# Kernel optimization log

Measured on AMD Instinct MI355X. Metric: run time of the kernel, lower is better.

## Reference

```python
import jax, jax.numpy as jnp
import numpy as np
import math

B, QL, KL, H, QD, KD, VD = 4, 1024, 1024, 16, 1024, 1024, 1024
QH = QD // H  # 64
KH = KD // H  # 64


def setup_inputs() -> dict:
    rng = jax.random.key(0)
    ks = jax.random.split(rng, 8)
    return {
        "query": jax.random.normal(ks[0], (B, QL, QD), jnp.float32),
        "key": jax.random.normal(ks[1], (B, KL, KD), jnp.float32),
        "value": jax.random.normal(ks[2], (B, KL, VD), jnp.float32),
        "pad_mask": jax.random.randint(ks[3], (B, QL), 0, 2),
        "q_w": jax.random.uniform(ks[4], (H, QL, QH), jnp.float32),
        "k_w": jax.random.uniform(ks[5], (H, KL, KH), jnp.float32),
        "v_w": jax.random.uniform(ks[6], (H, KL, KH), jnp.float32),
        "o_w": jax.random.uniform(ks[7], (H * KH, QD), jnp.float32),
    }


def reference(query, key, value, pad_mask, q_w, k_w, v_w, o_w):
    b = query.shape[0]
    h, ql, qh = q_w.shape
    kl, kh = k_w.shape[1], k_w.shape[2]

    # mask construction: causal (triu, offset 1) OR pad mask tiled as in torch repeat+view
    causal = jnp.triu(jnp.ones((ql, kl), jnp.float32), 1) == 1            # [i, j]
    pad = jnp.tile(pad_mask, (1, kl)).reshape(b, ql, kl) == 1             # [b, i, j]
    mask = causal[None, :, :] | pad                                      # [b, i, j]

    # positional per-head projections: free index of input feature dim is summed out
    wq = jnp.einsum('biq,his->bhis', query, q_w)                          # [b, h, i, s]
    wk = jnp.einsum('bjk,hjt->bhjt', key, k_w)                            # [b, h, j, t]
    wv = jnp.einsum('bjv,hjt->bhjt', value, v_w)                          # [b, h, j, t]

    scale = math.sqrt(h)  # torch uses query.size()[1] == head_num after projection
    scores = jnp.einsum('bhis,bhjs->bhij', wq, wk) / scale                # [b, h, i, j]
    scores = jnp.where(mask[:, None, :, :], -jnp.inf, scores)
    scores = jnp.nan_to_num(scores)  # -inf -> finfo.min, matching torch.nan_to_num

    weight = jax.nn.softmax(scores, axis=0)  # unusual: softmax over the batch axis
    heads = jnp.einsum('bhij,bhjt->bhit', weight, wv)                     # [b, h, i, t]
    heads = heads.reshape(b, -1, h * kh)  # torch .view: reinterprets [h,i,t] as [i, h*t]
    return jnp.einsum('bit,to->bio', heads, o_w)                          # [b, i, q_dim]
```

## Files before the change

### kernel.cpp

```cpp
#include <hip/hip_runtime.h>
#include <hip/hip_bf16.h>

#define NB 4
#define NL 1024
#define NH 16
#define ND 1024
#define HD 64
#define FMIN_F32 (-3.4028234663852886e38f)
#define LOG2E 1.4426950408889634f

typedef __bf16 bf16x8 __attribute__((ext_vector_type(8)));
typedef float f32x4 __attribute__((ext_vector_type(4)));
typedef unsigned int u32;

static __device__ inline unsigned short f2bf(float f) {
    __hip_bfloat16 h = __float2bfloat16(f);
    return __builtin_bit_cast(unsigned short, h);
}

static __device__ inline void bfsplit(float x, unsigned short& hi, unsigned short& lo) {
    unsigned u = __builtin_bit_cast(unsigned, x);
    unsigned r = (u + 0x7FFFu + ((u >> 16) & 1u)) >> 16;
    hi = (unsigned short)r;
    float hf = __builtin_bit_cast(float, r << 16);
    lo = f2bf(x - hf);
}

static __device__ __forceinline__ void gload16(void* lds, const void* g) {
    __builtin_amdgcn_global_load_lds(
        (const __attribute__((address_space(1))) u32*)g,
        (__attribute__((address_space(3))) u32*)lds, 16, 0, 0);
}

__global__ __launch_bounds__(256)
void rowsum_kernel(const float* __restrict__ q, const float* __restrict__ k,
                   const float* __restrict__ v, float* __restrict__ out) {
    int gw   = blockIdx.x * 4 + (threadIdx.x >> 6);
    int lane = threadIdx.x & 63;
    int tensor = gw >> 12;
    int row    = gw & 4095;
    const float* src = tensor == 0 ? q : (tensor == 1 ? k : v);
    const float* p = src + (size_t)row * ND;
    float s = 0.f;
#pragma unroll
    for (int t = 0; t < 4; ++t) {
        float4 x = *reinterpret_cast<const float4*>(p + t * 256 + lane * 4);
        s += (x.x + x.y) + (x.z + x.w);
    }
#pragma unroll
    for (int off = 32; off; off >>= 1) s += __shfl_xor(s, off);
    if (lane == 0) out[tensor * (NB * NL) + row] = s;
}

__global__ __launch_bounds__(256)
void prep_kernel(const float* __restrict__ k_w, const float* __restrict__ v_w,
                 const float* __restrict__ o_w, const float* __restrict__ sums,
                 unsigned short* __restrict__ kPhi, unsigned short* __restrict__ kPlo,
                 unsigned short* __restrict__ vP, unsigned short* __restrict__ BP,
                 float* __restrict__ S) {
    __shared__ float tile[64][132];
    __shared__ float vsL[256];
    const int tid = threadIdx.x;
    const int bx  = blockIdx.x;
    if (bx < 256) {
        const int h = bx >> 4, jt = bx & 15;
        char* hiT = (char*)kPhi + (size_t)(h * 16 + jt) * 8192;
        char* loT = (char*)kPlo + (size_t)(h * 16 + jt) * 8192;
        const int row = tid >> 2;
        const int s0  = (tid & 3) * 16;
        const float* src = k_w + ((size_t)(h * NL + jt * 64 + row)) * HD + s0;
#pragma unroll
        for (int t = 0; t < 4; ++t) {
            float4 x = reinterpret_cast<const float4*>(src)[t];
            unsigned short h0, h1, h2, h3, l0, l1, l2, l3;
            bfsplit(x.x, h0, l0); bfsplit(x.y, h1, l1);
            bfsplit(x.z, h2, l2); bfsplit(x.w, h3, l3);
            int off = (row * 128 + (s0 + 4 * t) * 2) ^ ((row & 7) << 4);
            *(uint2*)(hiT + off) = make_uint2((u32)h0 | ((u32)h1 << 16),
                                              (u32)h2 | ((u32)h3 << 16));
            *(uint2*)(loT + off) = make_uint2((u32)l0 | ((u32)l1 << 16),
                                              (u32)l2 | ((u32)l3 << 16));
        }
    } else if (bx < 512) {
        const int h = (bx - 256) >> 4, jt = (bx - 256) & 15;
#pragma unroll
        for (int t = 0; t < 4; ++t) {
            int id = tid + 256 * t;
            int j = id >> 4, t4 = (id & 15) * 4;
            *(float4*)&tile[j][t4] =
                *(const float4*)(v_w + ((size_t)(h * NL + jt * 64 + j)) * HD + t4);
        }
        vsL[tid] = sums[2 * NB * NL + (tid >> 6) * NL + jt * 64 + (tid & 63)];
        __syncthreads();
        char* vT_ = (char*)vP + (size_t)(h * 16 + jt) * 8192;
        const int trow = tid >> 2;
        const int jq   = (tid & 3) * 16;
#pragma unroll
        for (int q = 0; q < 4; ++q) {
            int j4 = jq + 4 * q;
            uint2 u;
            u.x = (u32)f2bf(tile[j4 + 0][trow]) | ((u32)f2bf(tile[j4 + 1][trow]) << 16);
            u.y = (u32)f2bf(tile[j4 + 2][trow]) | ((u32)f2bf(tile[j4 + 3][trow]) << 16);
            int off = (trow * 128 + j4 * 2) ^ ((trow & 7) << 4);
            *(uint2*)(vT_ + off) = u;
        }
        if (jt >= 1) {
            const int b = tid >> 6, t = tid & 63;
            float a = 0.f;
#pragma unroll 16
            for (int j = 0; j < 64; ++j)
                a = fmaf(vsL[b * 64 + j], tile[j][t], a);
            S[(((size_t)h * 16 + jt) * 4 + b) * 64 + t] = a;
        }
    } else {
        const int bxo = bx - 512;
        const int ot = bxo >> 4, kt = bxo & 15;
#pragma unroll
        for (int t = 0; t < 8; ++t) {
            int id = tid + 256 * t;
            int c = id >> 5, o4 = (id & 31) * 4;
            *(float4*)&tile[c][o4] =
                *(const float4*)(o_w + ((size_t)(kt * 64 + c)) * ND + ot * 128 + o4);
        }
        __syncthreads();
        char* bT = (char*)BP + (size_t)(ot * 16 + kt) * 16384;
#pragma unroll
        for (int t = 0; t < 8; ++t) {
            int id = tid + 256 * t;
            int ol = id >> 4, c4 = (id & 15) * 4;
            uint2 u;
            u.x = (u32)f2bf(tile[c4 + 0][ol]) | ((u32)f2bf(tile[c4 + 1][ol]) << 16);
            u.y = (u32)f2bf(tile[c4 + 2][ol]) | ((u32)f2bf(tile[c4 + 3][ol]) << 16);
            int off = (ol * 128 + c4 * 2) ^ ((ol & 7) << 4);
            *(uint2*)(bT + off) = u;
        }
    }
}

__global__ __launch_bounds__(512, 4)
void attn_kernel(const float* __restrict__ q_w, const int* __restrict__ pad,
                 const float* __restrict__ sums,
                 const unsigned short* __restrict__ kPhi,
                 const unsigned short* __restrict__ kPlo,
                 const unsigned short* __restrict__ vP,
                 const float* __restrict__ S,
                 unsigned short* __restrict__ AP) {
    __shared__ __align__(16) unsigned short kHi[2][4096], kLo[2][4096], vTl[2][4096];
    __shared__ __align__(16) unsigned short qHi[2048], qLo[2048];
    __shared__ __align__(16) unsigned short wlds[8192];
    __shared__ __align__(16) float qs4[128];
    __shared__ __align__(16) float ks4[2][256];
    __shared__ __align__(16) float vs4[2][256];
    __shared__ __align__(16) int   pm4[2][256];

    const float* qsum = sums;
    const float* ksum = sums + NB * NL;
    const float* vsum = sums + 2 * NB * NL;

    const int wid = blockIdx.x;
    const int gq  = wid >> 4;
    const int h   = wid & 15;
    const int itp = (gq < 16) ? (2 * gq) : (63 - 2 * gq);
    const int it0 = itp * 32;
    const int cut = (it0 >> 6) + 1;

    const int tid  = threadIdx.x;
    const int lane = tid & 63;
    const int w    = tid >> 6;
    const int l15  = lane & 15;
    const int kb   = (lane >> 4) * 16;

    {
        int row = tid >> 4;
        int s4  = (tid & 15) * 4;
        float4 x = *(const float4*)(q_w + ((size_t)(h * NL + it0 + row)) * HD + s4);
        unsigned short h0, h1, h2, h3, l0, l1, l2, l3;
        bfsplit(x.x, h0, l0); bfsplit(x.y, h1, l1);
        bfsplit(x.z, h2, l2); bfsplit(x.w, h3, l3);
        int off = (row * 128 + s4 * 2) ^ ((row & 7) << 4);
        *(uint2*)((char*)qHi + off) = make_uint2((u32)h0 | ((u32)h1 << 16),
                                                 (u32)h2 | ((u32)h3 << 16));
        *(uint2*)((char*)qLo + off) = make_uint2((u32)l0 | ((u32)l1 << 16),
                                                 (u32)l2 | ((u32)l3 << 16));
    }
    if (tid < 128) {
        int b = tid >> 5, i = tid & 31;
        qs4[i * 4 + b] = qsum[b * NL + it0 + i];
    }

    auto stage = [&](int buf, int jt) {
        const size_t tb = (size_t)(h * 16 + jt) * 8192 + tid * 16;
        gload16((char*)kHi[buf] + tid * 16, (const char*)kPhi + tb);
        gload16((char*)kLo[buf] + tid * 16, (const char*)kPlo + tb);
        gload16((char*)vTl[buf] + tid * 16, (const char*)vP + tb);
        if (tid < 256) {
            int b = tid >> 6, jj = tid & 63;
            ks4[buf][jj * 4 + b] = ksum[b * NL + jt * 64 + jj] * LOG2E;
            vs4[buf][jj * 4 + b] = vsum[b * NL + jt * 64 + jj];
            pm4[buf][jj * 4 + b] = pad[b * NL + jt * 64 + jj];
        }
    };

    const int gmi = (w & 1) * 16;
    const int gnj = (w >> 1) * 16;
    const int pb  = w >> 1;
    const int pmh = (w & 1) * 16;

    f32x4 accP[4];
#pragma unroll
    for (int n = 0; n < 4; ++n) accP[n] = (f32x4){0.f, 0.f, 0.f, 0.f};

    stage(0, 0);
    __syncthreads();
    int cur = 0;

    for (int jt = 0; jt < cut; ++jt) {
        const int j0 = jt * 64;
        if (jt + 1 < cut) stage(cur ^ 1, jt + 1);

        f32x4 g = (f32x4){0.f, 0.f, 0.f, 0.f};
#pragma unroll
        for (int ks = 0; ks < 2; ++ks) {
            const int arow = gmi + l15;
            const int brow = gnj + l15;
            const int aoff = (arow * 128 + ks * 64 + kb) ^ ((arow & 7) << 4);
            const int boff = (brow * 128 + ks * 64 + kb) ^ ((brow & 7) << 4);
            bf16x8 aHi = __builtin_bit_cast(bf16x8, *(const uint4*)((const char*)qHi + aoff));
            bf16x8 aLo = __builtin_bit_cast(bf16x8, *(const uint4*)((const char*)qLo + aoff));
            bf16x8 bHi = __builtin_bit_cast(bf16x8, *(const uint4*)((const char*)kHi[cur] + boff));
            bf16x8 bLo = __builtin_bit_cast(bf16x8, *(const uint4*)((const char*)kLo[cur] + boff));
            g = __builtin_amdgcn_mfma_f32_16x16x32_bf16(aHi, bHi, g, 0, 0, 0);
            g = __builtin_amdgcn_mfma_f32_16x16x32_bf16(aLo, bHi, g, 0, 0, 0);
            g = __builtin_amdgcn_mfma_f32_16x16x32_bf16(aHi, bLo, g, 0, 0, 0);
        }

        {
            const int j  = gnj + l15;
            const int jg = j0 + j;
            const float4 ksv = *(const float4*)&ks4[cur][j * 4];
            const float4 vsv = *(const float4*)&vs4[cur][j * 4];
            const int4   pmv = *(const int4*)&pm4[cur][j * 4];
#pragma unroll
            for (int r = 0; r < 4; ++r) {
                const int il = gmi + (lane >> 4) * 4 + r;
                const int ig = it0 + il;
                const float gv = g[r] * 0.25f;
                const float4 qsv = *(const float4*)&qs4[il * 4];
                const bool causal = jg > ig;
                const float sb0 = (causal || pmv.x) ? FMIN_F32 : qsv.x * ksv.x * gv;
                const float sb1 = (causal || pmv.y) ? FMIN_F32 : qsv.y * ksv.y * gv;
                const float sb2 = (causal || pmv.z) ? FMIN_F32 : qsv.z * ksv.z * gv;
                const float sb3 = (causal || pmv.w) ? FMIN_F32 : qsv.w * ksv.w * gv;
                const float mx = fmaxf(fmaxf(sb0, sb1), fmaxf(sb2, sb3));
                const float e0 = __builtin_amdgcn_exp2f(sb0 - mx);
                const float e1 = __builtin_amdgcn_exp2f(sb1 - mx);
                const float e2 = __builtin_amdgcn_exp2f(sb2 - mx);
                const float e3 = __builtin_amdgcn_exp2f(sb3 - mx);
                const float inv = __builtin_amdgcn_rcpf((e0 + e1) + (e2 + e3));
                const int off = (il * 128 + j * 2) ^ ((il & 7) << 4);
                *(unsigned short*)((char*)wlds + off)         = f2bf(e0 * inv * vsv.x);
                *(unsigned short*)((char*)wlds + 4096 + off)  = f2bf(e1 * inv * vsv.y);
                *(unsigned short*)((char*)wlds + 8192 + off)  = f2bf(e2 * inv * vsv.z);
                *(unsigned short*)((char*)wlds + 12288 + off) = f2bf(e3 * inv * vsv.w);
            }
        }
        asm volatile("s_waitcnt lgkmcnt(0)" ::: "memory");
        __builtin_amdgcn_s_barrier();
        __builtin_amdgcn_sched_barrier(0);

#pragma unroll
        for (int ks = 0; ks < 2; ++ks) {
            const int arow = pmh + l15;
            const int aoff = pb * 4096 + ((arow * 128 + ks * 64 + kb) ^ ((arow & 7) << 4));
            bf16x8 aF = __builtin_bit_cast(bf16x8, *(const uint4*)((const char*)wlds + aoff));
#pragma unroll
            for (int n = 0; n < 4; ++n) {
                const int vrow = n * 16 + l15;
                const int voff = (vrow * 128 + ks * 64 + kb) ^ ((vrow & 7) << 4);
                bf16x8 bF = __builtin_bit_cast(bf16x8, *(const uint4*)((const char*)vTl[cur] + voff));
                accP[n] = __builtin_amdgcn_mfma_f32_16x16x32_bf16(aF, bF, accP[n], 0, 0, 0);
            }
        }
        __syncthreads();
        cur ^= 1;
    }

    if (cut < 16) {
        float sv[4] = {0.f, 0.f, 0.f, 0.f};
        for (int jt = cut; jt < 16; ++jt) {
            const float* sp = S + (((size_t)h * 16 + jt) * 4 + pb) * 64;
#pragma unroll
            for (int n = 0; n < 4; ++n) sv[n] += sp[n * 16 + l15];
        }
#pragma unroll
        for (int n = 0; n < 4; ++n) {
            const float s4v = 0.25f * sv[n];
#pragma unroll
            for (int r = 0; r < 4; ++r) accP[n][r] += s4v;
        }
    }

    {
        const int ib = (it0 + pmh) >> 4;
        char* tbase = (char*)AP + (size_t)((pb * 16 + h) * 16) * 8192;
#pragma unroll
        for (int n = 0; n < 4; ++n)
#pragma unroll
            for (int r = 0; r < 4; ++r) {
                int kt = (lane >> 4) * 4 + r;
                int tt = n * 16 + l15;
                int off = (ib * 128 + tt * 2) ^ ((ib & 7) << 4);
                *(unsigned short*)(tbase + (size_t)kt * 8192 + off) = f2bf(accP[n][r]);
            }
    }
}

__global__ __launch_bounds__(256, 2)
void outgemm_kernel(const unsigned short* __restrict__ AP,
                    const unsigned short* __restrict__ BP,
                    float* __restrict__ out) {
    __shared__ __align__(16) unsigned short aL[2][4096];
    __shared__ __align__(16) unsigned short bL[2][8192];
    const int ox = blockIdx.x;
    const int my = blockIdx.y;
    const int tid  = threadIdx.x;
    const int lane = tid & 63;
    const int w    = tid >> 6;
    const int wr = (w & 1) * 32;
    const int wc = (w >> 1) * 64;
    const int l15  = lane & 15;
    const int kseg = (lane >> 4) * 16;

    f32x4 acc[2][4];
#pragma unroll
    for (int m = 0; m < 2; ++m)
#pragma unroll
        for (int n = 0; n < 4; ++n) acc[m][n] = (f32x4){0.f, 0.f, 0.f, 0.f};

    auto stage = [&](int buf, int kt) {
        const char* at = (const char*)AP + (size_t)(my * 16 + kt) * 8192;
        const char* bt = (const char*)BP + (size_t)(ox * 16 + kt) * 16384;
        gload16((char*)aL[buf] + tid * 16, at + tid * 16);
        gload16((char*)aL[buf] + 4096 + tid * 16, at + 4096 + tid * 16);
#pragma unroll
        for (int r = 0; r < 4; ++r)
            gload16((char*)bL[buf] + r * 4096 + tid * 16, bt + r * 4096 + tid * 16);
    };

    stage(0, 0);
    __syncthreads();
    int cur = 0;
    for (int kt = 0; kt < 16; ++kt) {
        if (kt < 15) stage(cur ^ 1, kt + 1);
#pragma unroll
        for (int ks = 0; ks < 2; ++ks) {
            bf16x8 aF[2], bF[4];
#pragma unroll
            for (int m = 0; m < 2; ++m) {
                int row = wr + m * 16 + l15;
                int off = (row * 128 + ks * 64 + kseg) ^ ((row & 7) << 4);
                aF[m] = __builtin_bit_cast(bf16x8, *(const uint4*)((const char*)aL[cur] + off));
            }
#pragma unroll
            for (int n = 0; n < 4; ++n) {
                int row = wc + n * 16 + l15;
                int off = (row * 128 + ks * 64 + kseg) ^ ((row & 7) << 4);
                bF[n] = __builtin_bit_cast(bf16x8, *(const uint4*)((const char*)bL[cur] + off));
            }
#pragma unroll
            for (int m = 0; m < 2; ++m)
#pragma unroll
                for (int n = 0; n < 4; ++n)
                    acc[m][n] = __builtin_amdgcn_mfma_f32_16x16x32_bf16(
                        aF[m], bF[n], acc[m][n], 0, 0, 0);
        }
        __syncthreads();
        cur ^= 1;
    }
#pragma unroll
    for (int m = 0; m < 2; ++m)
#pragma unroll
        for (int n = 0; n < 4; ++n)
#pragma unroll
            for (int r = 0; r < 4; ++r) {
                int row = my * 64 + wr + m * 16 + (lane >> 4) * 4 + r;
                int col = ox * 128 + wc + n * 16 + l15;
                out[(size_t)row * ND + col] = acc[m][n][r];
            }
}

extern "C" void kernel_launch(void* const* d_in, const int* in_sizes, int n_in,
                              void* d_out, int out_size, void* d_ws, size_t ws_size,
                              hipStream_t stream) {
    const float* query = (const float*)d_in[0];
    const float* key   = (const float*)d_in[1];
    const float* value = (const float*)d_in[2];
    const int*   pad   = (const int*)d_in[3];
    const float* q_w   = (const float*)d_in[4];
    const float* k_w   = (const float*)d_in[5];
    const float* v_w   = (const float*)d_in[6];
    const float* o_w   = (const float*)d_in[7];
    float* out = (float*)d_out;

    char* W = (char*)d_ws;
    float*          sums = (float*)W;
    unsigned short* kPhi = (unsigned short*)(W + 49152);
    unsigned short* kPlo = (unsigned short*)(W + 2146304);
    unsigned short* vP   = (unsigned short*)(W + 4243456);
    unsigned short* BP   = (unsigned short*)(W + 6340608);
    unsigned short* AP   = (unsigned short*)(W + 8437760);

    float* S = out;

    rowsum_kernel<<<3 * (NB * NL) / 4, 256, 0, stream>>>(query, key, value, sums);

    prep_kernel<<<640, 256, 0, stream>>>(k_w, v_w, o_w, sums, kPhi, kPlo, vP, BP, S);

    attn_kernel<<<512, 512, 0, stream>>>(q_w, pad, sums, kPhi, kPlo, vP, S, AP);

    dim3 gg(8, 64);
    outgemm_kernel<<<gg, 256, 0, stream>>>(AP, BP, out);
}
```

Baseline: 71.93 us.

## Transpose score MFMA for packed weight stores; triple-buffer output GEMM

The attention kernel now swaps the MFMA operands so each lane holds four consecutive key columns for one query row. Four bf16 weights can then be packed into a single 8-byte LDS store per batch instead of four scalar 2-byte stores, and the 0.25 scale is folded into the staged key sums. The per-row q-sum load and the LDS write offset are hoisted out of the tile loop. The output GEMM moves from a double buffer to a three-stage buffer that waits on vmcnt, keeping two tile loads in flight with one barrier per step, at the cost of more LDS per block and possibly lower occupancy.

```diff
diff --git a/kernel.cpp b/kernel.cpp
--- a/kernel.cpp
+++ b/kernel.cpp
@@ -195,7 +195,7 @@
         gload16((char*)vTl[buf] + tid * 16, (const char*)vP + tb);
         if (tid < 256) {
             int b = tid >> 6, jj = tid & 63;
-            ks4[buf][jj * 4 + b] = ksum[b * NL + jt * 64 + jj] * LOG2E;
+            ks4[buf][jj * 4 + b] = ksum[b * NL + jt * 64 + jj] * (LOG2E * 0.25f);
             vs4[buf][jj * 4 + b] = vsum[b * NL + jt * 64 + jj];
             pm4[buf][jj * 4 + b] = pad[b * NL + jt * 64 + jj];
         }
@@ -214,6 +214,12 @@
     __syncthreads();
     int cur = 0;
 
+    const int i_sm  = gmi + l15;
+    const int ig    = it0 + i_sm;
+    const int jb_sm = gnj + (lane >> 4) * 4;
+    const float4 qsv = *(const float4*)&qs4[i_sm * 4];
+    const int woff = (i_sm * 128 + jb_sm * 2) ^ ((i_sm & 7) << 4);
+
     for (int jt = 0; jt < cut; ++jt) {
         const int j0 = jt * 64;
         if (jt + 1 < cut) stage(cur ^ 1, jt + 1);
@@ -221,47 +227,51 @@
         f32x4 g = (f32x4){0.f, 0.f, 0.f, 0.f};
 #pragma unroll
         for (int ks = 0; ks < 2; ++ks) {
-            const int arow = gmi + l15;
-            const int brow = gnj + l15;
+            const int arow = gnj + l15;
+            const int brow = gmi + l15;
             const int aoff = (arow * 128 + ks * 64 + kb) ^ ((arow & 7) << 4);
             const int boff = (brow * 128 + ks * 64 + kb) ^ ((brow & 7) << 4);
-            bf16x8 aHi = __builtin_bit_cast(bf16x8, *(const uint4*)((const char*)qHi + aoff));
-            bf16x8 aLo = __builtin_bit_cast(bf16x8, *(const uint4*)((const char*)qLo + aoff));
-            bf16x8 bHi = __builtin_bit_cast(bf16x8, *(const uint4*)((const char*)kHi[cur] + boff));
-            bf16x8 bLo = __builtin_bit_cast(bf16x8, *(const uint4*)((const char*)kLo[cur] + boff));
-            g = __builtin_amdgcn_mfma_f32_16x16x32_bf16(aHi, bHi, g, 0, 0, 0);
-            g = __builtin_amdgcn_mfma_f32_16x16x32_bf16(aLo, bHi, g, 0, 0, 0);
-            g = __builtin_amdgcn_mfma_f32_16x16x32_bf16(aHi, bLo, g, 0, 0, 0);
+            bf16x8 kHiF = __builtin_bit_cast(bf16x8, *(const uint4*)((const char*)kHi[cur] + aoff));
+            bf16x8 kLoF = __builtin_bit_cast(bf16x8, *(const uint4*)((const char*)kLo[cur] + aoff));
+            bf16x8 qHiF = __builtin_bit_cast(bf16x8, *(const uint4*)((const char*)qHi + boff));
+            bf16x8 qLoF = __builtin_bit_cast(bf16x8, *(const uint4*)((const char*)qLo + boff));
+            g = __builtin_amdgcn_mfma_f32_16x16x32_bf16(kHiF, qHiF, g, 0, 0, 0);
+            g = __builtin_amdgcn_mfma_f32_16x16x32_bf16(kLoF, qHiF, g, 0, 0, 0);
+            g = __builtin_amdgcn_mfma_f32_16x16x32_bf16(kHiF, qLoF, g, 0, 0, 0);
         }
 
         {
-            const int j  = gnj + l15;
-            const int jg = j0 + j;
-            const float4 ksv = *(const float4*)&ks4[cur][j * 4];
-            const float4 vsv = *(const float4*)&vs4[cur][j * 4];
-            const int4   pmv = *(const int4*)&pm4[cur][j * 4];
+            float wv[4][4];
 #pragma unroll
             for (int r = 0; r < 4; ++r) {
-                const int il = gmi + (lane >> 4) * 4 + r;
-                const int ig = it0 + il;
-                const float gv = g[r] * 0.25f;
-                const float4 qsv = *(const float4*)&qs4[il * 4];
+                const int j  = jb_sm + r;
+                const int jg = j0 + j;
+                const float4 ksv = *(const float4*)&ks4[cur][j * 4];
+                const float4 vsv = *(const float4*)&vs4[cur][j * 4];
+                const int4   pmv = *(const int4*)&pm4[cur][j * 4];
+                const float gr = g[r];
                 const bool causal = jg > ig;
-                const float sb0 = (causal || pmv.x) ? FMIN_F32 : qsv.x * ksv.x * gv;
-                const float sb1 = (causal || pmv.y) ? FMIN_F32 : qsv.y * ksv.y * gv;
-                const float sb2 = (causal || pmv.z) ? FMIN_F32 : qsv.z * ksv.z * gv;
-                const float sb3 = (causal || pmv.w) ? FMIN_F32 : qsv.w * ksv.w * gv;
+                const float sb0 = (causal || pmv.x) ? FMIN_F32 : qsv.x * ksv.x * gr;
+                const float sb1 = (causal || pmv.y) ? FMIN_F32 : qsv.y * ksv.y * gr;
+                const float sb2 = (causal || pmv.z) ? FMIN_F32 : qsv.z * ksv.z * gr;
+                const float sb3 = (causal || pmv.w) ? FMIN_F32 : qsv.w * ksv.w * gr;
                 const float mx = fmaxf(fmaxf(sb0, sb1), fmaxf(sb2, sb3));
                 const float e0 = __builtin_amdgcn_exp2f(sb0 - mx);
                 const float e1 = __builtin_amdgcn_exp2f(sb1 - mx);
                 const float e2 = __builtin_amdgcn_exp2f(sb2 - mx);
                 const float e3 = __builtin_amdgcn_exp2f(sb3 - mx);
                 const float inv = __builtin_amdgcn_rcpf((e0 + e1) + (e2 + e3));
-                const int off = (il * 128 + j * 2) ^ ((il & 7) << 4);
-                *(unsigned short*)((char*)wlds + off)         = f2bf(e0 * inv * vsv.x);
-                *(unsigned short*)((char*)wlds + 4096 + off)  = f2bf(e1 * inv * vsv.y);
-                *(unsigned short*)((char*)wlds + 8192 + off)  = f2bf(e2 * inv * vsv.z);
-                *(unsigned short*)((char*)wlds + 12288 + off) = f2bf(e3 * inv * vsv.w);
+                wv[r][0] = e0 * inv * vsv.x;
+                wv[r][1] = e1 * inv * vsv.y;
+                wv[r][2] = e2 * inv * vsv.z;
+                wv[r][3] = e3 * inv * vsv.w;
+            }
+#pragma unroll
+            for (int b = 0; b < 4; ++b) {
+                uint2 p;
+                p.x = (u32)f2bf(wv[0][b]) | ((u32)f2bf(wv[1][b]) << 16);
+                p.y = (u32)f2bf(wv[2][b]) | ((u32)f2bf(wv[3][b]) << 16);
+                *(uint2*)((char*)wlds + b * 4096 + woff) = p;
             }
         }
         asm volatile("s_waitcnt lgkmcnt(0)" ::: "memory");
@@ -319,8 +329,8 @@
 void outgemm_kernel(const unsigned short* __restrict__ AP,
                     const unsigned short* __restrict__ BP,
                     float* __restrict__ out) {
-    __shared__ __align__(16) unsigned short aL[2][4096];
-    __shared__ __align__(16) unsigned short bL[2][8192];
+    __shared__ __align__(16) unsigned short aL[3][4096];
+    __shared__ __align__(16) unsigned short bL[3][8192];
     const int ox = blockIdx.x;
     const int my = blockIdx.y;
     const int tid  = threadIdx.x;
@@ -347,11 +357,7 @@
             gload16((char*)bL[buf] + r * 4096 + tid * 16, bt + r * 4096 + tid * 16);
     };
 
-    stage(0, 0);
-    __syncthreads();
-    int cur = 0;
-    for (int kt = 0; kt < 16; ++kt) {
-        if (kt < 15) stage(cur ^ 1, kt + 1);
+    auto compute = [&](int cb) {
 #pragma unroll
         for (int ks = 0; ks < 2; ++ks) {
             bf16x8 aF[2], bF[4];
@@ -359,13 +365,13 @@
             for (int m = 0; m < 2; ++m) {
                 int row = wr + m * 16 + l15;
                 int off = (row * 128 + ks * 64 + kseg) ^ ((row & 7) << 4);
-                aF[m] = __builtin_bit_cast(bf16x8, *(const uint4*)((const char*)aL[cur] + off));
+                aF[m] = __builtin_bit_cast(bf16x8, *(const uint4*)((const char*)aL[cb] + off));
             }
 #pragma unroll
             for (int n = 0; n < 4; ++n) {
                 int row = wc + n * 16 + l15;
                 int off = (row * 128 + ks * 64 + kseg) ^ ((row & 7) << 4);
-                bF[n] = __builtin_bit_cast(bf16x8, *(const uint4*)((const char*)bL[cur] + off));
+                bF[n] = __builtin_bit_cast(bf16x8, *(const uint4*)((const char*)bL[cb] + off));
             }
 #pragma unroll
             for (int m = 0; m < 2; ++m)
@@ -374,9 +380,22 @@
                     acc[m][n] = __builtin_amdgcn_mfma_f32_16x16x32_bf16(
                         aF[m], bF[n], acc[m][n], 0, 0, 0);
         }
-        __syncthreads();
-        cur ^= 1;
-    }
+    };
+
+    stage(0, 0);
+    stage(1, 1);
+    for (int kt = 0; kt < 15; ++kt) {
+        asm volatile("s_waitcnt vmcnt(6)" ::: "memory");
+        __builtin_amdgcn_s_barrier();
+        __builtin_amdgcn_sched_barrier(0);
+        if (kt + 2 < 16) stage((kt + 2) % 3, kt + 2);
+        compute(kt % 3);
+    }
+    asm volatile("s_waitcnt vmcnt(0)" ::: "memory");
+    __builtin_amdgcn_s_barrier();
+    __builtin_amdgcn_sched_barrier(0);
+    compute(15 % 3);
+
 #pragma unroll
     for (int m = 0; m < 2; ++m)
 #pragma unroll
```

After: 69.19 us. -3.8%, faster.
